# Kernel optimization log

Measured on AMD Instinct MI355X. Metric: run time of the kernel, lower is better.

## Reference

```python
import jax, jax.numpy as jnp
import numpy as np

B = 32768   # batch
D0 = 64     # node-0 feature dim
D1 = 64     # node-1 feature dim
M = 8       # modules per node
H = 256     # hidden width
O0 = 128    # node-0 output width
O1 = 32     # final output width
B_INIT = 0.1
INIT_W = 0.003


def _fanin_uniform(key, shape):
    bound = 1.0 / np.sqrt(shape[-2])
    return jax.random.uniform(key, shape, jnp.float32, -bound, bound)


def setup_inputs() -> dict:
    key = jax.random.key(0)
    ks = jax.random.split(key, 10)
    feat = jax.random.normal(ks[0], (B, D0 + D1), jnp.float32)
    a0 = jax.random.randint(ks[1], (B,), 0, M)
    a1 = jax.random.randint(ks[2], (B,), 0, M)
    oh0 = jax.nn.one_hot(a0, M, dtype=jnp.float32)
    oh1 = jax.nn.one_hot(a1, M, dtype=jnp.float32)
    input_val = jnp.concatenate([feat, oh0, oh1], axis=1)  # [B, 144]
    # node 0 (all post-interface, hidden init + ReLU on both layers since graph_depth < last)
    W00 = _fanin_uniform(ks[3], (M, D0, H)); b00 = jnp.full((M, H), B_INIT, jnp.float32)
    W01 = _fanin_uniform(ks[4], (M, H, O0)); b01 = jnp.full((M, O0), B_INIT, jnp.float32)
    # node 1 pre-interface (layer i=0)
    W1p = _fanin_uniform(ks[5], (M, D1, H)); b1p = jnp.full((M, H), B_INIT, jnp.float32)
    # node 1 post-interface layer i=1: input = node0_out (128) concat pre (256) = 384
    W1a = _fanin_uniform(ks[6], (M, O0 + H, O0)); b1a = jnp.full((M, O0), B_INIT, jnp.float32)
    # node 1 output layer i=2: uniform(-init_w, init_w), Identity activation
    W1o = jax.random.uniform(ks[7], (M, O0, O1), jnp.float32, -INIT_W, INIT_W)
    b1o = jax.random.uniform(ks[8], (M, O1), jnp.float32, -INIT_W, INIT_W)
    return {"input_val": input_val, "W00": W00, "b00": b00, "W01": W01, "b01": b01,
            "W1p": W1p, "b1p": b1p, "W1a": W1a, "b1a": b1a, "W1o": W1o, "b1o": b1o}


def _routed(x, W, b, onehot, act):
    # per-module linear for all modules, then one-hot select the assigned module per sample
    y = jnp.einsum('bi,mio->bmo', x, W) + b          # [B, M, out]
    y = jnp.einsum('bmo,bm->bo', y, onehot)           # [B, out]
    return jax.nn.relu(y) if act else y


def reference(input_val, W00, b00, W01, b01, W1p, b1p, W1a, b1a, W1o, b1o):
    feat0 = input_val[:, :D0]
    feat1 = input_val[:, D0:D0 + D1]
    oh0 = input_val[:, D0 + D1:D0 + D1 + M]
    oh1 = input_val[:, D0 + D1 + M:D0 + D1 + 2 * M]
    # graph depth 0, node 0: post-interface MLP (ReLU on both layers)
    h = _routed(feat0, W00, b00, oh0, True)
    h = _routed(h, W01, b01, oh0, True)               # [B, O0]
    # graph depth 1, node 1: pre-interface, concat prev-depth output, post-interface
    g = _routed(feat1, W1p, b1p, oh1, True)           # [B, H]
    g = _routed(jnp.concatenate([h, g], axis=-1), W1a, b1a, oh1, True)  # [B, O0]
    out = _routed(g, W1o, b1o, oh1, False)            # [B, O1], Identity output activation
    return out
```

## Files before the change

### kernel.cpp

```cpp
#include <hip/hip_runtime.h>
#include <hip/hip_bf16.h>

#define BATCH 32768
#define NPAIR 64
#define NBLK  128

typedef __bf16 bf16x8 __attribute__((ext_vector_type(8)));
typedef float  f32x4  __attribute__((ext_vector_type(4)));
typedef float  f32x4e __attribute__((ext_vector_type(4)));
static_assert(sizeof(bf16x8) == 16, "bf16x8 must be 16B");

#define WS_CNT      0
#define WS_BASE     256
#define WS_BH       1024
#define WS_PAIR     66560
#define WS_ROWLIST  197632
#define WS_WF00     336896
#define WS_WF01     599040
#define WS_WF1P     1123328
#define WS_WF1A     1385472
#define WS_WF1O     2171904

__device__ __forceinline__ unsigned short f2bf(float x) {
  __bf16 h = (__bf16)x;
  return __builtin_bit_cast(unsigned short, h);
}

#define KEEP(x) asm volatile("" : "+v"(x))

__global__ __launch_bounds__(256) void k_combo(const float* __restrict__ w00,
                                               const float* __restrict__ w01,
                                               const float* __restrict__ w1p,
                                               const float* __restrict__ w1a,
                                               const float* __restrict__ w1o,
                                               const float* __restrict__ inp,
                                               char* __restrict__ ws) {
  __shared__ unsigned short lds[64 * 72];
  int bid = blockIdx.x;
  if (bid >= 240) {
    int* h = (int*)lds;
    int rbid = bid - 240;
    int t = threadIdx.x;
    if (t < NPAIR) h[t] = 0;
    __syncthreads();
    int r = rbid * 256 + t;
    const float* q = inp + (size_t)r * 144 + 128;
    float4 u0 = *(const float4*)(q + 0);
    float4 u1 = *(const float4*)(q + 4);
    float4 v0 = *(const float4*)(q + 8);
    float4 v1 = *(const float4*)(q + 12);
    int a0 = 0;
    if (u0.y > 0.5f) a0 = 1; if (u0.z > 0.5f) a0 = 2; if (u0.w > 0.5f) a0 = 3;
    if (u1.x > 0.5f) a0 = 4; if (u1.y > 0.5f) a0 = 5; if (u1.z > 0.5f) a0 = 6; if (u1.w > 0.5f) a0 = 7;
    int a1 = 0;
    if (v0.y > 0.5f) a1 = 1; if (v0.z > 0.5f) a1 = 2; if (v0.w > 0.5f) a1 = 3;
    if (v1.x > 0.5f) a1 = 4; if (v1.y > 0.5f) a1 = 5; if (v1.z > 0.5f) a1 = 6; if (v1.w > 0.5f) a1 = 7;
    int p = a0 * 8 + a1;
    ((int*)(ws + WS_PAIR))[r] = p;
    atomicAdd(&h[p], 1);
    __syncthreads();
    if (t < NPAIR) ((int*)(ws + WS_BH))[rbid * NPAIR + t] = h[t];
    return;
  }
  const float* src; char* dst; int I, O, lt, NT, KC;
  if (bid < 32)       { src = w00; dst = ws + WS_WF00; I = 64;  O = 256; lt = bid;       NT = 16; KC = 2; }
  else if (bid < 96)  { src = w01; dst = ws + WS_WF01; I = 256; O = 128; lt = bid - 32;  NT = 8;  KC = 8; }
  else if (bid < 128) { src = w1p; dst = ws + WS_WF1P; I = 64;  O = 256; lt = bid - 96;  NT = 16; KC = 2; }
  else if (bid < 224) { src = w1a; dst = ws + WS_WF1A; I = 384; O = 128; lt = bid - 128; NT = 8;  KC = 12; }
  else                { src = w1o; dst = ws + WS_WF1O; I = 128; O = 32;  lt = bid - 224; NT = 2;  KC = 4; }
  int tI = I >> 6;
  int tO = (O + 63) >> 6;
  int m   = lt / (tI * tO);
  int rem = lt % (tI * tO);
  int ib = rem / tO, ob = rem % tO;
  int tx = threadIdx.x & 63, ty = threadIdx.x >> 6;
  const float* s = src + (size_t)m * I * O;
  #pragma unroll 4
  for (int s4 = 0; s4 < 16; ++s4) {
    int li = s4 * 4 + ty;
    int o  = ob * 64 + tx;
    float v = (o < O) ? s[(size_t)(ib * 64 + li) * O + o] : 0.f;
    lds[li * 72 + tx] = f2bf(v);
  }
  __syncthreads();
  int lane = threadIdx.x & 63, u = threadIdx.x >> 6;
  int ln = lane & 15, lq = lane >> 4;
  #pragma unroll
  for (int it = 0; it < 2; ++it) {
    int fi  = it * 4 + u;
    int ntl = fi >> 1, kcl = fi & 1;
    int ntg = ob * 4 + ntl, kcg = ib * 2 + kcl;
    if (ntg * 16 < O) {
      bf16x8 f;
      #pragma unroll
      for (int j = 0; j < 8; ++j)
        f[j] = __builtin_bit_cast(__bf16, lds[(kcl * 32 + lq * 8 + j) * 72 + ntl * 16 + ln]);
      *(bf16x8*)(dst + (((size_t)(m * NT + ntg) * KC + kcg) * 64 + lane) * 16) = f;
    }
  }
}

__global__ __launch_bounds__(256) void k_part(const int* __restrict__ bh,
                                              const int* __restrict__ pairArr,
                                              int* __restrict__ cnt,
                                              int* __restrict__ base,
                                              int* __restrict__ rowlist) {
  __shared__ int lbh[NBLK * NPAIR];
  __shared__ int loff[NPAIR];
  __shared__ int h[NPAIR];
  int tid = threadIdx.x, bid = blockIdx.x;
  const int4* s4 = (const int4*)bh;
  int4* d4 = (int4*)lbh;
  #pragma unroll
  for (int i = 0; i < 8; ++i) d4[tid + i * 256] = s4[tid + i * 256];
  if (tid < NPAIR) h[tid] = 0;
  __syncthreads();
  if (tid < NPAIR) {
    int c = 0, partial = 0;
    for (int b = 0; b < NBLK; ++b) {
      int v = lbh[b * NPAIR + tid];
      if (b < bid) partial += v;
      c += v;
    }
    int ntp = (c + 31) >> 5;
    int z = ntp;
    #pragma unroll
    for (int d = 1; d < 64; d <<= 1) { int y = __shfl_up(z, d); if (tid >= d) z += y; }
    int pbase = (z - ntp) * 32;
    loff[tid] = pbase + partial;
    if (bid == 0) { cnt[tid] = c; base[tid] = pbase; }
  }
  __syncthreads();
  int r = bid * 256 + tid;
  int p = pairArr[r];
  int rank = atomicAdd(&h[p], 1);
  rowlist[loff[p] + rank] = r;
}

__global__ __launch_bounds__(512, 1) void k_fused(
    const float* __restrict__ inp,
    const float* __restrict__ b00, const float* __restrict__ b01,
    const float* __restrict__ b1p, const float* __restrict__ b1a,
    const float* __restrict__ b1o,
    const char* __restrict__ ws, float* __restrict__ out)
{
  __shared__ char smem[155648];
  unsigned short* G   = (unsigned short*)(smem + 98304);
  unsigned short* H1m = (unsigned short*)(smem + 114688);
  unsigned short* HO  = (unsigned short*)(smem + 131072);
  unsigned short* G2  = (unsigned short*)(smem + 139264);
  char*           xs  = smem + 147456;

  int p     = blockIdx.x >> 2;
  int slice = blockIdx.x & 3;
  int e0 = p >> 3, e1 = p & 7;
  int cnt = ((const int*)(ws + WS_CNT))[p];
  int pbase = ((const int*)(ws + WS_BASE))[p];
  int ntp = (cnt + 31) >> 5;
  if (slice >= ntp) return;
  const int* rlbase = (const int*)(ws + WS_ROWLIST) + pbase;

  int tid  = threadIdx.x;
  {
    const f32x4e* s1 = (const f32x4e*)(ws + WS_WF1A + (size_t)e1 * 98304);
    f32x4e* d1 = (f32x4e*)smem;
    #pragma unroll
    for (int i = 0; i < 12; ++i) d1[tid + i * 512] = s1[tid + i * 512];
  }

  int lane = tid & 63;
  int w    = tid >> 6;
  int ln = lane & 15, lq = lane >> 4;
  int kcol = lq * 8;

  bf16x8 w00f[2][2], w1pf[2][2];
  #pragma unroll
  for (int nt = 0; nt < 2; ++nt)
    #pragma unroll
    for (int kc = 0; kc < 2; ++kc) {
      w00f[nt][kc] = *(const bf16x8*)(ws + WS_WF00 + (size_t)e0 * 32768 +
                                      ((((w * 2 + nt) * 2 + kc) * 64 + lane) << 4));
      w1pf[nt][kc] = *(const bf16x8*)(ws + WS_WF1P + (size_t)e1 * 32768 +
                                      ((((w * 2 + nt) * 2 + kc) * 64 + lane) << 4));
    }
  bf16x8 wc[8];
  #pragma unroll
  for (int kc = 0; kc < 8; ++kc)
    wc[kc] = *(const bf16x8*)(ws + WS_WF01 + (size_t)e0 * 65536 +
                              (((w * 8 + kc) * 64 + lane) << 4));
  bf16x8 wo[4];
  if (w < 4) {
    #pragma unroll
    for (int kc = 0; kc < 4; ++kc)
      wo[kc] = *(const bf16x8*)(ws + WS_WF1O + (size_t)e1 * 8192 +
                                ((((w >> 1) * 4 + kc) * 64 + lane) << 4));
  }
  #pragma unroll
  for (int nt = 0; nt < 2; ++nt)
    #pragma unroll
    for (int kc = 0; kc < 2; ++kc) { KEEP(w00f[nt][kc]); KEEP(w1pf[nt][kc]); }
  #pragma unroll
  for (int kc = 0; kc < 8; ++kc) KEEP(wc[kc]);
  if (w < 4) {
    #pragma unroll
    for (int kc = 0; kc < 4; ++kc) KEEP(wo[kc]);
  }

  float bias00[2], bias1p[2];
  #pragma unroll
  for (int nt = 0; nt < 2; ++nt) {
    bias00[nt] = b00[e0 * 256 + w * 32 + nt * 16 + ln];
    bias1p[nt] = b1p[e1 * 256 + w * 32 + nt * 16 + ln];
  }
  float bias01 = b01[e0 * 128 + w * 16 + ln];
  float bias1a = b1a[e1 * 128 + w * 16 + ln];
  float bias1o = (w < 4) ? b1o[e1 * 32 + (w >> 1) * 16 + ln] : 0.f;

  const f32x4 z4 = {0.f, 0.f, 0.f, 0.f};
  int srow = tid >> 5, scol = tid & 31;

  {
    int nr0 = min(32, cnt - slice * 32);
    const int* rl0 = rlbase + slice * 32;
    #pragma unroll
    for (int pass = 0; pass < 2; ++pass) {
      int row = pass * 16 + srow;
      int rg = (row < nr0) ? rl0[row] : -1;
      ushort4 v8 = {0, 0, 0, 0};
      if (rg >= 0) {
        f32x4e u = __builtin_nontemporal_load(
            (const f32x4e*)(inp + (size_t)rg * 144 + scol * 4));
        v8.x = f2bf(u.x); v8.y = f2bf(u.y); v8.z = f2bf(u.z); v8.w = f2bf(u.w);
      }
      int byte = (row * 256 + scol * 8) ^ ((row & 7) << 4);
      *(ushort4*)(xs + byte) = v8;
    }
  }
  __syncthreads();

  for (int t = slice; t < ntp; t += 4) {
    int nr = min(32, cnt - t * 32);
    const int* rl = rlbase + t * 32;

    int t2 = t + 4;
    bool hasNext = (t2 < ntp);
    f32x4e pre[2];
    #pragma unroll
    for (int pass = 0; pass < 2; ++pass) { pre[pass].x = 0; pre[pass].y = 0; pre[pass].z = 0; pre[pass].w = 0; }
    if (hasNext) {
      int nr2 = min(32, cnt - t2 * 32);
      const int* rl2 = rlbase + t2 * 32;
      #pragma unroll
      for (int pass = 0; pass < 2; ++pass) {
        int row = pass * 16 + srow;
        int rg = (row < nr2) ? rl2[row] : -1;
        if (rg >= 0)
          pre[pass] = __builtin_nontemporal_load(
              (const f32x4e*)(inp + (size_t)rg * 144 + scol * 4));
      }
      KEEP(pre[0]); KEEP(pre[1]);
    }

    bf16x8 axf[2][2][2];
    #pragma unroll
    for (int half = 0; half < 2; ++half)
      #pragma unroll
      for (int mt = 0; mt < 2; ++mt)
        #pragma unroll
        for (int kc = 0; kc < 2; ++kc) {
          int row = mt * 16 + ln;
          int byte = (row * 256 + half * 128 + kc * 64 + lq * 16) ^ ((row & 7) << 4);
          axf[half][mt][kc] = *(const bf16x8*)(xs + byte);
        }
    #pragma unroll
    for (int nt = 0; nt < 2; ++nt) {
      int n = w * 32 + nt * 16 + ln;
      f32x4 acc0[2] = {z4, z4}, acc1[2] = {z4, z4};
      #pragma unroll
      for (int kc = 0; kc < 2; ++kc)
        #pragma unroll
        for (int mt = 0; mt < 2; ++mt) {
          acc0[mt] = __builtin_amdgcn_mfma_f32_16x16x32_bf16(axf[0][mt][kc], w00f[nt][kc], acc0[mt], 0, 0, 0);
          acc1[mt] = __builtin_amdgcn_mfma_f32_16x16x32_bf16(axf[1][mt][kc], w1pf[nt][kc], acc1[mt], 0, 0, 0);
        }
      #pragma unroll
      for (int mt = 0; mt < 2; ++mt)
        #pragma unroll
        for (int r = 0; r < 4; ++r) {
          int row = mt * 16 + lq * 4 + r;
          int sw = ((n << 1) ^ ((row & 7) << 4));
          H1m[(row * 512 + sw) >> 1] = f2bf(fmaxf(acc0[mt][r] + bias00[nt], 0.f));
          G  [(row * 512 + sw) >> 1] = f2bf(fmaxf(acc1[mt][r] + bias1p[nt], 0.f));
        }
    }
    __syncthreads();

    if (hasNext) {
      #pragma unroll
      for (int pass = 0; pass < 2; ++pass) {
        int row = pass * 16 + srow;
        ushort4 v8;
        v8.x = f2bf(pre[pass].x); v8.y = f2bf(pre[pass].y);
        v8.z = f2bf(pre[pass].z); v8.w = f2bf(pre[pass].w);
        int byte = (row * 256 + scol * 8) ^ ((row & 7) << 4);
        *(ushort4*)(xs + byte) = v8;
      }
    }

    f32x4 acc1a[2] = {z4, z4};
    {
      f32x4 acc[2] = {z4, z4};
      #pragma unroll
      for (int kc = 0; kc < 8; ++kc) {
        #pragma unroll
        for (int mt = 0; mt < 2; ++mt) {
          int row = mt * 16 + ln;
          bf16x8 afr = *(const bf16x8*)&H1m[(row * 512 + (((kc * 32 + kcol) << 1) ^ ((row & 7) << 4))) >> 1];
          acc[mt] = __builtin_amdgcn_mfma_f32_16x16x32_bf16(afr, wc[kc], acc[mt], 0, 0, 0);
        }
        {
          int kcg = kc + 4;
          bf16x8 bfr = *(const bf16x8*)(smem + (((w * 12 + kcg) * 64 + lane) << 4));
          #pragma unroll
          for (int mt = 0; mt < 2; ++mt) {
            int row = mt * 16 + ln;
            bf16x8 afr = *(const bf16x8*)&G[(row * 512 + (((kc * 32 + kcol) << 1) ^ ((row & 7) << 4))) >> 1];
            acc1a[mt] = __builtin_amdgcn_mfma_f32_16x16x32_bf16(afr, bfr, acc1a[mt], 0, 0, 0);
          }
        }
      }
      int n = w * 16 + ln;
      #pragma unroll
      for (int mt = 0; mt < 2; ++mt)
        #pragma unroll
        for (int r = 0; r < 4; ++r) {
          int row = mt * 16 + lq * 4 + r;
          float v = fmaxf(acc[mt][r] + bias01, 0.f);
          HO[(row * 256 + ((n << 1) ^ ((row & 7) << 4))) >> 1] = f2bf(v);
        }
    }
    __syncthreads();

    {
      #pragma unroll
      for (int kc = 0; kc < 4; ++kc) {
        bf16x8 bfr = *(const bf16x8*)(smem + (((w * 12 + kc) * 64 + lane) << 4));
        #pragma unroll
        for (int mt = 0; mt < 2; ++mt) {
          int row = mt * 16 + ln;
          bf16x8 afr = *(const bf16x8*)&HO[(row * 256 + (((kc * 32 + kcol) << 1) ^ ((row & 7) << 4))) >> 1];
          acc1a[mt] = __builtin_amdgcn_mfma_f32_16x16x32_bf16(afr, bfr, acc1a[mt], 0, 0, 0);
        }
      }
      int n = w * 16 + ln;
      #pragma unroll
      for (int mt = 0; mt < 2; ++mt)
        #pragma unroll
        for (int r = 0; r < 4; ++r) {
          int row = mt * 16 + lq * 4 + r;
          float v = fmaxf(acc1a[mt][r] + bias1a, 0.f);
          G2[(row * 256 + ((n << 1) ^ ((row & 7) << 4))) >> 1] = f2bf(v);
        }
    }
    __syncthreads();

    if (w < 4) {
      int mt = w & 1;
      int n  = (w >> 1) * 16 + ln;
      f32x4 acc = z4;
      #pragma unroll
      for (int kc = 0; kc < 4; ++kc) {
        int row = mt * 16 + ln;
        bf16x8 afr = *(const bf16x8*)&G2[(row * 256 + (((kc * 32 + kcol) << 1) ^ ((row & 7) << 4))) >> 1];
        acc = __builtin_amdgcn_mfma_f32_16x16x32_bf16(afr, wo[kc], acc, 0, 0, 0);
      }
      #pragma unroll
      for (int r = 0; r < 4; ++r) {
        int row = mt * 16 + lq * 4 + r;
        if (row < nr) {
          int rg = rl[row];
          __builtin_nontemporal_store(acc[r] + bias1o, &out[(size_t)rg * 32 + n]);
        }
      }
    }
  }
}

extern "C" void kernel_launch(void* const* d_in, const int* in_sizes, int n_in,
                              void* d_out, int out_size, void* d_ws, size_t ws_size,
                              hipStream_t stream) {
  const float* inp = (const float*)d_in[0];
  const float* w00 = (const float*)d_in[1];
  const float* b00 = (const float*)d_in[2];
  const float* w01 = (const float*)d_in[3];
  const float* b01 = (const float*)d_in[4];
  const float* w1p = (const float*)d_in[5];
  const float* b1p = (const float*)d_in[6];
  const float* w1a = (const float*)d_in[7];
  const float* b1a = (const float*)d_in[8];
  const float* w1o = (const float*)d_in[9];
  const float* b1o = (const float*)d_in[10];
  char*  ws  = (char*)d_ws;
  float* out = (float*)d_out;

  k_combo<<<368, 256, 0, stream>>>(w00, w01, w1p, w1a, w1o, inp, ws);
  k_part<<<NBLK, 256, 0, stream>>>((const int*)(ws + WS_BH),
                                   (const int*)(ws + WS_PAIR),
                                   (int*)(ws + WS_CNT), (int*)(ws + WS_BASE),
                                   (int*)(ws + WS_ROWLIST));
  k_fused<<<256, 512, 0, stream>>>(inp, b00, b01, b1p, b1a, b1o, ws, out);
}
```

Before: 44.90 us.

## Shrink shared memory and registers to double fused-kernel grid and occupancy

Launches 512 blocks with 8 slices per expert pair instead of 256 with 4. To make that fit, LDS drops from about 152KB to 80KB: only the low K-chunks of W1a stay in shared memory, the high chunks move to registers, and HO and G2 share one buffer behind an added barrier. W01 and W1o fragments are now read from global memory inside the tile loop instead of being kept in registers. The aim is more resident blocks and more parallelism per pair, at the cost of repeated global/L2 weight loads per tile and an extra synchronisation.

New measurement: 90.85 us. 102% more time.

```diff
diff --git a/kernel.cpp b/kernel.cpp
--- a/kernel.cpp
+++ b/kernel.cpp
@@ -137,22 +137,22 @@
   rowlist[loff[p] + rank] = r;
 }
 
-__global__ __launch_bounds__(512, 1) void k_fused(
+__global__ __launch_bounds__(512, 4) void k_fused(
     const float* __restrict__ inp,
     const float* __restrict__ b00, const float* __restrict__ b01,
     const float* __restrict__ b1p, const float* __restrict__ b1a,
     const float* __restrict__ b1o,
     const char* __restrict__ ws, float* __restrict__ out)
 {
-  __shared__ char smem[155648];
-  unsigned short* G   = (unsigned short*)(smem + 98304);
-  unsigned short* H1m = (unsigned short*)(smem + 114688);
-  unsigned short* HO  = (unsigned short*)(smem + 131072);
-  unsigned short* G2  = (unsigned short*)(smem + 139264);
-  char*           xs  = smem + 147456;
-
-  int p     = blockIdx.x >> 2;
-  int slice = blockIdx.x & 3;
+  __shared__ char smem[81920];
+  unsigned short* G   = (unsigned short*)(smem + 32768);
+  unsigned short* H1m = (unsigned short*)(smem + 49152);
+  unsigned short* HO  = (unsigned short*)(smem + 65536);
+  unsigned short* G2  = (unsigned short*)(smem + 65536);
+  char*           xs  = smem + 73728;
+
+  int p     = blockIdx.x >> 3;
+  int slice = blockIdx.x & 7;
   int e0 = p >> 3, e1 = p & 7;
   int cnt = ((const int*)(ws + WS_CNT))[p];
   int pbase = ((const int*)(ws + WS_BASE))[p];
@@ -165,7 +165,12 @@
     const f32x4e* s1 = (const f32x4e*)(ws + WS_WF1A + (size_t)e1 * 98304);
     f32x4e* d1 = (f32x4e*)smem;
     #pragma unroll
-    for (int i = 0; i < 12; ++i) d1[tid + i * 512] = s1[tid + i * 512];
+    for (int i = 0; i < 4; ++i) {
+      int fidx = tid + i * 512;
+      int chunk = fidx >> 6, within = fidx & 63;
+      int w2 = chunk >> 2, kc = chunk & 3;
+      d1[fidx] = s1[(w2 * 12 + kc) * 64 + within];
+    }
   }
 
   int lane = tid & 63;
@@ -183,28 +188,17 @@
       w1pf[nt][kc] = *(const bf16x8*)(ws + WS_WF1P + (size_t)e1 * 32768 +
                                       ((((w * 2 + nt) * 2 + kc) * 64 + lane) << 4));
     }
-  bf16x8 wc[8];
-  #pragma unroll
-  for (int kc = 0; kc < 8; ++kc)
-    wc[kc] = *(const bf16x8*)(ws + WS_WF01 + (size_t)e0 * 65536 +
-                              (((w * 8 + kc) * 64 + lane) << 4));
-  bf16x8 wo[4];
-  if (w < 4) {
-    #pragma unroll
-    for (int kc = 0; kc < 4; ++kc)
-      wo[kc] = *(const bf16x8*)(ws + WS_WF1O + (size_t)e1 * 8192 +
-                                ((((w >> 1) * 4 + kc) * 64 + lane) << 4));
-  }
+  bf16x8 wa_hi[8];
+  #pragma unroll
+  for (int j = 0; j < 8; ++j)
+    wa_hi[j] = *(const bf16x8*)(ws + WS_WF1A + (size_t)e1 * 98304 +
+                                (((w * 12 + 4 + j) * 64 + lane) << 4));
   #pragma unroll
   for (int nt = 0; nt < 2; ++nt)
     #pragma unroll
     for (int kc = 0; kc < 2; ++kc) { KEEP(w00f[nt][kc]); KEEP(w1pf[nt][kc]); }
   #pragma unroll
-  for (int kc = 0; kc < 8; ++kc) KEEP(wc[kc]);
-  if (w < 4) {
-    #pragma unroll
-    for (int kc = 0; kc < 4; ++kc) KEEP(wo[kc]);
-  }
+  for (int j = 0; j < 8; ++j) KEEP(wa_hi[j]);
 
   float bias00[2], bias1p[2];
   #pragma unroll
@@ -238,11 +232,11 @@
   }
   __syncthreads();
 
-  for (int t = slice; t < ntp; t += 4) {
+  for (int t = slice; t < ntp; t += 8) {
     int nr = min(32, cnt - t * 32);
     const int* rl = rlbase + t * 32;
 
-    int t2 = t + 4;
+    int t2 = t + 8;
     bool hasNext = (t2 < ntp);
     f32x4e pre[2];
     #pragma unroll
@@ -312,21 +306,19 @@
       f32x4 acc[2] = {z4, z4};
       #pragma unroll
       for (int kc = 0; kc < 8; ++kc) {
+        bf16x8 bfr01 = *(const bf16x8*)(ws + WS_WF01 + (size_t)e0 * 65536 +
+                                        (((w * 8 + kc) * 64 + lane) << 4));
         #pragma unroll
         for (int mt = 0; mt < 2; ++mt) {
           int row = mt * 16 + ln;
           bf16x8 afr = *(const bf16x8*)&H1m[(row * 512 + (((kc * 32 + kcol) << 1) ^ ((row & 7) << 4))) >> 1];
-          acc[mt] = __builtin_amdgcn_mfma_f32_16x16x32_bf16(afr, wc[kc], acc[mt], 0, 0, 0);
-        }
-        {
-          int kcg = kc + 4;
-          bf16x8 bfr = *(const bf16x8*)(smem + (((w * 12 + kcg) * 64 + lane) << 4));
-          #pragma unroll
-          for (int mt = 0; mt < 2; ++mt) {
-            int row = mt * 16 + ln;
-            bf16x8 afr = *(const bf16x8*)&G[(row * 512 + (((kc * 32 + kcol) << 1) ^ ((row & 7) << 4))) >> 1];
-            acc1a[mt] = __builtin_amdgcn_mfma_f32_16x16x32_bf16(afr, bfr, acc1a[mt], 0, 0, 0);
-          }
+          acc[mt] = __builtin_amdgcn_mfma_f32_16x16x32_bf16(afr, bfr01, acc[mt], 0, 0, 0);
+        }
+        #pragma unroll
+        for (int mt = 0; mt < 2; ++mt) {
+          int row = mt * 16 + ln;
+          bf16x8 afr = *(const bf16x8*)&G[(row * 512 + (((kc * 32 + kcol) << 1) ^ ((row & 7) << 4))) >> 1];
+          acc1a[mt] = __builtin_amdgcn_mfma_f32_16x16x32_bf16(afr, wa_hi[kc], acc1a[mt], 0, 0, 0);
         }
       }
       int n = w * 16 + ln;
@@ -344,7 +336,7 @@
     {
       #pragma unroll
       for (int kc = 0; kc < 4; ++kc) {
-        bf16x8 bfr = *(const bf16x8*)(smem + (((w * 12 + kc) * 64 + lane) << 4));
+        bf16x8 bfr = *(const bf16x8*)(smem + (((w * 4 + kc) * 64 + lane) << 4));
         #pragma unroll
         for (int mt = 0; mt < 2; ++mt) {
           int row = mt * 16 + ln;
@@ -352,6 +344,9 @@
           acc1a[mt] = __builtin_amdgcn_mfma_f32_16x16x32_bf16(afr, bfr, acc1a[mt], 0, 0, 0);
         }
       }
+    }
+    __syncthreads();
+    {
       int n = w * 16 + ln;
       #pragma unroll
       for (int mt = 0; mt < 2; ++mt)
@@ -372,7 +367,9 @@
       for (int kc = 0; kc < 4; ++kc) {
         int row = mt * 16 + ln;
         bf16x8 afr = *(const bf16x8*)&G2[(row * 256 + (((kc * 32 + kcol) << 1) ^ ((row & 7) << 4))) >> 1];
-        acc = __builtin_amdgcn_mfma_f32_16x16x32_bf16(afr, wo[kc], acc, 0, 0, 0);
+        bf16x8 bfr = *(const bf16x8*)(ws + WS_WF1O + (size_t)e1 * 8192 +
+                                      ((((w >> 1) * 4 + kc) * 64 + lane) << 4));
+        acc = __builtin_amdgcn_mfma_f32_16x16x32_bf16(afr, bfr, acc, 0, 0, 0);
       }
       #pragma unroll
       for (int r = 0; r < 4; ++r) {
@@ -408,5 +405,5 @@
                                    (const int*)(ws + WS_PAIR),
                                    (int*)(ws + WS_CNT), (int*)(ws + WS_BASE),
                                    (int*)(ws + WS_ROWLIST));
-  k_fused<<<256, 512, 0, stream>>>(inp, b00, b01, b1p, b1a, b1o, ws, out);
+  k_fused<<<512, 512, 0, stream>>>(inp, b00, b01, b1p, b1a, b1o, ws, out);
 }
```
